# Performance work log

Measured on AMD Instinct MI355X. Metric: run time of the kernel, lower is better.

## Reference

```python
import jax, jax.numpy as jnp
import numpy as np

N_NODES = 50000
N_EDGES = 800000
IN_DIM = 128
EMB = 64
EDGE_DIM = 6
N_LAYERS = 4
OUT_DIM = 1


def setup_inputs() -> dict:
    key = jax.random.key(0)
    ks = jax.random.split(key, 20)
    s = 0.05
    inp = {
        "x": jax.random.normal(ks[0], (N_NODES, IN_DIM), jnp.float32),
        "edge_index": jax.random.randint(ks[1], (2, N_EDGES), 0, N_NODES, jnp.int64),
        "edge_attr": jax.random.normal(ks[2], (N_EDGES, EDGE_DIM), jnp.float32),
        # input projection
        "lin_in_w": jax.random.normal(ks[3], (IN_DIM, EMB), jnp.float32) * s,
        "lin_in_b": jnp.zeros((EMB,), jnp.float32),
        # stacked per-layer MLP params: message MLP psi: (2*EMB+EDGE_DIM)->EMB->EMB
        "msg_w1": jax.random.normal(ks[4], (N_LAYERS, 2 * EMB + EDGE_DIM, EMB), jnp.float32) * s,
        "msg_b1": jnp.zeros((N_LAYERS, EMB), jnp.float32),
        "msg_w2": jax.random.normal(ks[5], (N_LAYERS, EMB, EMB), jnp.float32) * s,
        "msg_b2": jnp.zeros((N_LAYERS, EMB), jnp.float32),
        # update MLP phi: (2*EMB)->EMB->EMB
        "upd_w1": jax.random.normal(ks[6], (N_LAYERS, 2 * EMB, EMB), jnp.float32) * s,
        "upd_b1": jnp.zeros((N_LAYERS, EMB), jnp.float32),
        "upd_w2": jax.random.normal(ks[7], (N_LAYERS, EMB, EMB), jnp.float32) * s,
        "upd_b2": jnp.zeros((N_LAYERS, EMB), jnp.float32),
        # output head
        "pred_w": jax.random.normal(ks[8], (EMB, OUT_DIM), jnp.float32) * s,
        "pred_b": jnp.zeros((OUT_DIM,), jnp.float32),
    }
    return inp


def reference(x, edge_index, edge_attr, lin_in_w, lin_in_b,
              msg_w1, msg_b1, msg_w2, msg_b2,
              upd_w1, upd_b1, upd_w2, upd_b2,
              pred_w, pred_b):
    n = x.shape[0]
    src = edge_index[0]  # h_j: source nodes
    dst = edge_index[1]  # h_i: target nodes (aggregation index in PyG default flow)
    h = x @ lin_in_w + lin_in_b  # (n, EMB)
    n_layers = msg_w1.shape[0]
    for l in range(n_layers):
        # message: psi([h_i, h_j, e_ij])  -> (E, EMB)
        m = jnp.concatenate([h[dst], h[src], edge_attr], axis=-1)
        m = jax.nn.relu(m @ msg_w1[l] + msg_b1[l])
        m = jax.nn.relu(m @ msg_w2[l] + msg_b2[l])
        # aggregate: scatter-add over target nodes
        agg = jax.ops.segment_sum(m, dst, num_segments=n)
        # update: phi([h, m_i]) with residual connection (h = h + conv(h))
        u = jnp.concatenate([h, agg], axis=-1)
        u = jax.nn.relu(u @ upd_w1[l] + upd_b1[l])
        u = jax.nn.relu(u @ upd_w2[l] + upd_b2[l])
        h = h + u
    out = h @ pred_w + pred_b  # (n, OUT_DIM)
    return jnp.sum(out, axis=-2)  # (OUT_DIM,)
```

## Files before the change

kernel.cpp:

```cpp
#include <hip/hip_runtime.h>


typedef __attribute__((ext_vector_type(8))) short short8;
typedef __attribute__((ext_vector_type(4))) float float4v;

__device__ __forceinline__ unsigned short f2bf(float f) {
    unsigned int u = __float_as_uint(f);
    unsigned int r = u + 0x7fff + ((u >> 16) & 1);
    return (unsigned short)(r >> 16);
}
__device__ __forceinline__ float bf2f(unsigned short u) {
    return __uint_as_float(((unsigned int)u) << 16);
}

#define MFMA16(a, b, c) __builtin_amdgcn_mfma_f32_16x16x32_bf16(a, b, c, 0, 0, 0)

struct bfpair { short hi, lo; };
__device__ __forceinline__ bfpair wsplit(float wv) {
    bfpair p;
    unsigned short h = f2bf(wv);
    float hf = __uint_as_float(((unsigned int)h) << 16);
    p.hi = (short)h;
    p.lo = (short)f2bf(wv - hf);
    return p;
}

#define WP_TOTAL 106496
#define OFF_IN   0
#define OFF_PRE(l)  (8192  + (l) * 8192)
#define OFF_MW2(l)  (40960 + (l) * 4096)
#define OFF_UW1(l)  (57344 + (l) * 8192)
#define OFF_UW2(l)  (90112 + (l) * 4096)

__global__ __launch_bounds__(256) void k_wprep(const float* __restrict__ lin_w,
        const float* __restrict__ mw1, const float* __restrict__ mw2,
        const float* __restrict__ uw1, const float* __restrict__ uw2,
        unsigned short* __restrict__ H, unsigned short* __restrict__ L) {
    const int tid = blockIdx.x * 256 + threadIdx.x;
    if (tid >= WP_TOTAL) return;
    float val;
    if (tid < 8192) {
        int rem = tid;
        int nt = rem >> 11, kf = (rem >> 9) & 3;
        int lane = (rem >> 3) & 63, j = rem & 7;
        int k = kf * 32 + (lane >> 4) * 8 + j;
        val = lin_w[k * 64 + nt * 16 + (lane & 15)];
    } else if (tid < 40960) {
        int t = tid - 8192, layer = t >> 13, rem = t & 8191;
        int nt = rem >> 10, kf = (rem >> 9) & 1;
        int lane = (rem >> 3) & 63, j = rem & 7;
        int k = kf * 32 + (lane >> 4) * 8 + j;
        const float* w1 = mw1 + (size_t)layer * 134 * 64;
        val = (nt < 4) ? w1[k * 64 + nt * 16 + (lane & 15)]
                       : w1[(64 + k) * 64 + (nt - 4) * 16 + (lane & 15)];
    } else if (tid < 57344) {
        int t = tid - 40960, layer = t >> 12, rem = t & 4095;
        int nt = rem >> 10, kf = (rem >> 9) & 1;
        int lane = (rem >> 3) & 63, j = rem & 7;
        int k = kf * 32 + (lane >> 4) * 8 + j;
        val = mw2[(size_t)layer * 4096 + k * 64 + nt * 16 + (lane & 15)];
    } else if (tid < 90112) {
        int t = tid - 57344, layer = t >> 13, rem = t & 8191;
        int nt = rem >> 11, kf = (rem >> 9) & 3;
        int lane = (rem >> 3) & 63, j = rem & 7;
        int k = kf * 32 + (lane >> 4) * 8 + j;
        val = uw1[(size_t)layer * 8192 + k * 64 + nt * 16 + (lane & 15)];
    } else {
        int t = tid - 90112, layer = t >> 12, rem = t & 4095;
        int nt = rem >> 10, kf = (rem >> 9) & 1;
        int lane = (rem >> 3) & 63, j = rem & 7;
        int k = kf * 32 + (lane >> 4) * 8 + j;
        val = uw2[(size_t)layer * 4096 + k * 64 + nt * 16 + (lane & 15)];
    }
    bfpair p = wsplit(val);
    H[tid] = (unsigned short)p.hi;
    L[tid] = (unsigned short)p.lo;
}

#define LOADFRAG(dst, arr, nt, KF, kf) \
    dst = *(const short8*)&arr[((((nt) * (KF)) + (kf)) * 64 + lane) * 8]

__global__ __launch_bounds__(256) void k_hist(const int* __restrict__ dst,
        int* __restrict__ deg, int nEdges) {
    int e = blockIdx.x * blockDim.x + threadIdx.x;
    if (e < nEdges) atomicAdd(&deg[dst[e]], 1);
}

__global__ __launch_bounds__(256) void k_scan1(const int* __restrict__ deg,
        int* __restrict__ local, int* __restrict__ bsum, int nNodes) {
    __shared__ int sm[256];
    const int t = threadIdx.x;
    const int n = blockIdx.x * 256 + t;
    int v = (n < nNodes) ? deg[n] : 0;
    sm[t] = v;
    __syncthreads();
    for (int off = 1; off < 256; off <<= 1) {
        int u = (t >= off) ? sm[t - off] : 0;
        __syncthreads();
        sm[t] += u;
        __syncthreads();
    }
    if (n < nNodes) local[n] = sm[t] - v;
    if (t == 255) bsum[blockIdx.x] = sm[255];
}

__global__ __launch_bounds__(256) void k_scan2(int* __restrict__ bsum, int nB) {
    __shared__ int sm[256];
    const int t = threadIdx.x;
    int v = (t < nB) ? bsum[t] : 0;
    sm[t] = v;
    __syncthreads();
    for (int off = 1; off < 256; off <<= 1) {
        int u = (t >= off) ? sm[t - off] : 0;
        __syncthreads();
        sm[t] += u;
        __syncthreads();
    }
    if (t < nB) bsum[t] = sm[t] - v;
}

__global__ __launch_bounds__(256) void k_scan3(const int* __restrict__ local,
        const int* __restrict__ bsum, int* __restrict__ cursor, int nNodes) {
    int n = blockIdx.x * 256 + threadIdx.x;
    if (n < nNodes) cursor[n] = bsum[blockIdx.x] + local[n];
}

__global__ __launch_bounds__(256) void k_scatter(const int* __restrict__ src,
        const int* __restrict__ dst, const float* __restrict__ ea,
        int* __restrict__ cursor, int* __restrict__ col_src,
        int* __restrict__ dst_s, float* __restrict__ ea_s, int nEdges) {
    int e = blockIdx.x * blockDim.x + threadIdx.x;
    if (e < nEdges) {
        int d = dst[e];
        int pos = atomicAdd(&cursor[d], 1);
        col_src[pos] = src[e];
        dst_s[pos] = d;
        const float* p = ea + (size_t)e * 6;
        float* q = ea_s + (size_t)pos * 6;
#pragma unroll
        for (int j = 0; j < 6; ++j) q[j] = p[j];
    }
}


__global__ __launch_bounds__(256) void k_in(const float* __restrict__ x,
        const unsigned short* __restrict__ wh, const unsigned short* __restrict__ wl,
        const float* __restrict__ bia, float* __restrict__ h, int nNodes) {
    const int lane = threadIdx.x & 63;
    const int wib  = threadIdx.x >> 6;
    const int quad = lane >> 4, col = lane & 15;
    __shared__ unsigned short sm[4][16 * 136];
    unsigned short* __restrict__ mt = sm[wib];

    short8 bh[4][4], bl[4][4];
#pragma unroll
    for (int nt = 0; nt < 4; ++nt)
#pragma unroll
        for (int kf = 0; kf < 4; ++kf) {
            LOADFRAG(bh[nt][kf], wh, nt, 4, kf);
            LOADFRAG(bl[nt][kf], wl, nt, 4, kf);
        }
    float bv[4];
#pragma unroll
    for (int nt = 0; nt < 4; ++nt) bv[nt] = bia[nt * 16 + col];

    const int nTiles = (nNodes + 15) >> 4;
    const int wid = blockIdx.x * 4 + wib;
    const int nw  = gridDim.x * 4;
    for (int tile = wid; tile < nTiles; tile += nw) {
        const int base = tile * 16;
#pragma unroll
        for (int j = 0; j < 16; ++j) {
            int row = min(base + j, nNodes - 1);
            mt[j * 136 + lane]      = f2bf(x[(size_t)row * 128 + lane]);
            mt[j * 136 + 64 + lane] = f2bf(x[(size_t)row * 128 + 64 + lane]);
        }
        __builtin_amdgcn_s_waitcnt(0);
        short8 a[4];
#pragma unroll
        for (int kf = 0; kf < 4; ++kf)
            a[kf] = *(const short8*)&mt[col * 136 + kf * 32 + quad * 8];
#pragma unroll
        for (int nt = 0; nt < 4; ++nt) {
            float4v c = {0.f, 0.f, 0.f, 0.f};
#pragma unroll
            for (int kf = 0; kf < 4; ++kf) c = MFMA16(a[kf], bh[nt][kf], c);
#pragma unroll
            for (int kf = 0; kf < 4; ++kf) c = MFMA16(a[kf], bl[nt][kf], c);
#pragma unroll
            for (int r = 0; r < 4; ++r) {
                int row = base + quad * 4 + r;
                if (row < nNodes)
                    h[(size_t)row * 64 + nt * 16 + col] = c[r] + bv[nt];
            }
        }
    }
}

__global__ __launch_bounds__(256) void k_pre(const float* __restrict__ h,
        const unsigned short* __restrict__ wh, const unsigned short* __restrict__ wl,
        const float* __restrict__ b1m,
        unsigned short* __restrict__ P, unsigned short* __restrict__ Q,
        int nNodes) {
    const int lane = threadIdx.x & 63;
    const int wib  = threadIdx.x >> 6;
    const int quad = lane >> 4, col = lane & 15;
    __shared__ unsigned short sm[4][16 * 72];
    unsigned short* __restrict__ mt = sm[wib];

    short8 bh[8][2], bl[8][2];
#pragma unroll
    for (int nt = 0; nt < 8; ++nt)
#pragma unroll
        for (int kf = 0; kf < 2; ++kf) {
            LOADFRAG(bh[nt][kf], wh, nt, 2, kf);
            LOADFRAG(bl[nt][kf], wl, nt, 2, kf);
        }
    float bv1[4];
#pragma unroll
    for (int nt = 0; nt < 4; ++nt) bv1[nt] = b1m[nt * 16 + col];

    const int nTiles = (nNodes + 15) >> 4;
    const int wid = blockIdx.x * 4 + wib;
    const int nw  = gridDim.x * 4;
    for (int tile = wid; tile < nTiles; tile += nw) {
        const int base = tile * 16;
#pragma unroll
        for (int j = 0; j < 16; ++j) {
            int row = min(base + j, nNodes - 1);
            mt[j * 72 + lane] = f2bf(h[(size_t)row * 64 + lane]);
        }
        __builtin_amdgcn_s_waitcnt(0);
        short8 a0 = *(const short8*)&mt[col * 72 + quad * 8];
        short8 a1 = *(const short8*)&mt[col * 72 + 32 + quad * 8];
#pragma unroll
        for (int nt = 0; nt < 8; ++nt) {
            float4v c = {0.f, 0.f, 0.f, 0.f};
            c = MFMA16(a0, bh[nt][0], c);
            c = MFMA16(a1, bh[nt][1], c);
            c = MFMA16(a0, bl[nt][0], c);
            c = MFMA16(a1, bl[nt][1], c);
            unsigned short* __restrict__ outp = (nt < 4) ? P : Q;
            const int nc = (nt & 3) * 16 + col;
            const float badd = (nt < 4) ? bv1[nt & 3] : 0.f;
#pragma unroll
            for (int r = 0; r < 4; ++r) {
                int row = base + quad * 4 + r;
                if (row < nNodes) outp[(size_t)row * 64 + nc] = f2bf(c[r] + badd);
            }
        }
    }
}

__global__ __launch_bounds__(256) void k_upd1(const float* __restrict__ h,
        const float* __restrict__ agg,
        const unsigned short* __restrict__ wh, const unsigned short* __restrict__ wl,
        const float* __restrict__ b1, float* __restrict__ tv, int nNodes) {
    const int lane = threadIdx.x & 63;
    const int wib  = threadIdx.x >> 6;
    const int quad = lane >> 4, col = lane & 15;
    __shared__ unsigned short sm[4][16 * 136];
    unsigned short* __restrict__ mt = sm[wib];

    short8 bh[4][4], bl[4][4];
#pragma unroll
    for (int nt = 0; nt < 4; ++nt)
#pragma unroll
        for (int kf = 0; kf < 4; ++kf) {
            LOADFRAG(bh[nt][kf], wh, nt, 4, kf);
            LOADFRAG(bl[nt][kf], wl, nt, 4, kf);
        }
    float bv[4];
#pragma unroll
    for (int nt = 0; nt < 4; ++nt) bv[nt] = b1[nt * 16 + col];

    const int nTiles = (nNodes + 15) >> 4;
    const int wid = blockIdx.x * 4 + wib;
    const int nw  = gridDim.x * 4;
    for (int tile = wid; tile < nTiles; tile += nw) {
        const int base = tile * 16;
#pragma unroll
        for (int j = 0; j < 16; ++j) {
            int row = min(base + j, nNodes - 1);
            mt[j * 136 + lane]      = f2bf(h[(size_t)row * 64 + lane]);
            mt[j * 136 + 64 + lane] = f2bf(agg[(size_t)row * 64 + lane]);
        }
        __builtin_amdgcn_s_waitcnt(0);
        short8 a[4];
#pragma unroll
        for (int kf = 0; kf < 4; ++kf)
            a[kf] = *(const short8*)&mt[col * 136 + kf * 32 + quad * 8];
#pragma unroll
        for (int nt = 0; nt < 4; ++nt) {
            float4v c = {0.f, 0.f, 0.f, 0.f};
#pragma unroll
            for (int kf = 0; kf < 4; ++kf) c = MFMA16(a[kf], bh[nt][kf], c);
#pragma unroll
            for (int kf = 0; kf < 4; ++kf) c = MFMA16(a[kf], bl[nt][kf], c);
#pragma unroll
            for (int r = 0; r < 4; ++r) {
                int row = base + quad * 4 + r;
                if (row < nNodes)
                    tv[(size_t)row * 64 + nt * 16 + col] = fmaxf(c[r] + bv[nt], 0.f);
            }
        }
    }
}

__global__ __launch_bounds__(256) void k_upd2(float* __restrict__ h,
        float* __restrict__ tv,
        const unsigned short* __restrict__ wh, const unsigned short* __restrict__ wl,
        const float* __restrict__ b2, float* __restrict__ colsum,
        int nNodes, int doCS) {
    const int lane = threadIdx.x & 63;
    const int wib  = threadIdx.x >> 6;
    const int quad = lane >> 4, col = lane & 15;
    __shared__ unsigned short sm[4][16 * 72];
    unsigned short* __restrict__ mt = sm[wib];

    short8 bh[4][2], bl[4][2];
#pragma unroll
    for (int nt = 0; nt < 4; ++nt)
#pragma unroll
        for (int kf = 0; kf < 2; ++kf) {
            LOADFRAG(bh[nt][kf], wh, nt, 2, kf);
            LOADFRAG(bl[nt][kf], wl, nt, 2, kf);
        }
    float bv[4];
#pragma unroll
    for (int nt = 0; nt < 4; ++nt) bv[nt] = b2[nt * 16 + col];

    float cs0 = 0.f, cs1 = 0.f, cs2 = 0.f, cs3 = 0.f;
    const int nTiles = (nNodes + 15) >> 4;
    const int wid = blockIdx.x * 4 + wib;
    const int nw  = gridDim.x * 4;
    for (int tile = wid; tile < nTiles; tile += nw) {
        const int base = tile * 16;
#pragma unroll
        for (int j = 0; j < 16; ++j) {
            int row = min(base + j, nNodes - 1);
            mt[j * 72 + lane] = f2bf(tv[(size_t)row * 64 + lane]);
        }
        __builtin_amdgcn_s_waitcnt(0);
#pragma unroll
        for (int j = 0; j < 16; ++j) {
            int row = base + j;
            if (row < nNodes) tv[(size_t)row * 64 + lane] = 0.f;
        }
        short8 a0 = *(const short8*)&mt[col * 72 + quad * 8];
        short8 a1 = *(const short8*)&mt[col * 72 + 32 + quad * 8];
#pragma unroll
        for (int nt = 0; nt < 4; ++nt) {
            float4v c = {0.f, 0.f, 0.f, 0.f};
            c = MFMA16(a0, bh[nt][0], c);
            c = MFMA16(a1, bh[nt][1], c);
            c = MFMA16(a0, bl[nt][0], c);
            c = MFMA16(a1, bl[nt][1], c);
#pragma unroll
            for (int r = 0; r < 4; ++r) {
                int row = base + quad * 4 + r;
                if (row < nNodes) {
                    float* hp = &h[(size_t)row * 64 + nt * 16 + col];
                    float hn = *hp + fmaxf(c[r] + bv[nt], 0.f);
                    *hp = hn;
                    cs0 += (nt == 0) ? hn : 0.f;
                    cs1 += (nt == 1) ? hn : 0.f;
                    cs2 += (nt == 2) ? hn : 0.f;
                    cs3 += (nt == 3) ? hn : 0.f;
                }
            }
        }
    }
    if (doCS) {
        cs0 += __shfl_xor(cs0, 16); cs0 += __shfl_xor(cs0, 32);
        cs1 += __shfl_xor(cs1, 16); cs1 += __shfl_xor(cs1, 32);
        cs2 += __shfl_xor(cs2, 16); cs2 += __shfl_xor(cs2, 32);
        cs3 += __shfl_xor(cs3, 16); cs3 += __shfl_xor(cs3, 32);
        const float tot = (quad == 0) ? cs0 : (quad == 1) ? cs1
                        : (quad == 2) ? cs2 : cs3;
        atomicAdd(&colsum[lane], tot);
    }
}

#define EST 72

__global__ __launch_bounds__(256, 4) void k_edge(const unsigned short* __restrict__ P,
        const unsigned short* __restrict__ Q, const float* __restrict__ ea_s,
        const int* __restrict__ col_src, const int* __restrict__ dst_s,
        const float* __restrict__ w1e,
        const unsigned short* __restrict__ wh, const unsigned short* __restrict__ wl,
        const float* __restrict__ b2,
        float* __restrict__ agg, int nEdges) {
    const int lane = threadIdx.x & 63;
    const int wib  = threadIdx.x >> 6;
    const int wid  = blockIdx.x * 4 + wib;
    const int nw   = gridDim.x * 4;
    const int quad = lane >> 4;
    const int col  = lane & 15;
    const int li   = lane & 31;

    __shared__ unsigned short m1b[4][32 * EST];
    __shared__ unsigned short wB[8192];
    unsigned short* __restrict__ mt = m1b[wib];

    {
        const short8* __restrict__ sH = (const short8*)wh;
        const short8* __restrict__ sL = (const short8*)wl;
        short8* __restrict__ dB = (short8*)wB;
        for (int i = threadIdx.x; i < 512; i += 256) {
            dB[i]       = sH[i];
            dB[512 + i] = sL[i];
        }
    }
    __syncthreads();

    float w1ec[6];
#pragma unroll
    for (int j = 0; j < 6; ++j) w1ec[j] = w1e[j * 64 + lane];

    float b2v[4];
#pragma unroll
    for (int nt = 0; nt < 4; ++nt) b2v[nt] = b2[nt * 16 + col];

    const int nBatch = (nEdges + 31) >> 5;
    const int per = nBatch / nw, rem = nBatch % nw;
    const int btLo = wid * per + min(wid, rem);
    const int btHi = btLo + per + (wid < rem ? 1 : 0);

    for (int bt = btLo; bt < btHi; ++bt) {
        const int base = __builtin_amdgcn_readfirstlane(bt << 5);
        const int gidx = min(base + li, nEdges - 1);
        const int vdj = dst_s[gidx];
        const int vsj = col_src[gidx];
        const int vprev = __shfl_up(vdj, 1);
        unsigned long long bmask =
            __ballot(lane < 32 && (li == 0 || vdj != vprev));
        bmask |= (1ull << 32) | 1ull;

#pragma unroll
        for (int j = 0; j < 32; ++j) {
            const int d = __builtin_amdgcn_readlane(vdj, j);
            const int s = __builtin_amdgcn_readlane(vsj, j);
            const int idx = min(base + j, nEdges - 1);
            float t = bf2f(P[(size_t)d * 64 + lane]) +
                      bf2f(Q[(size_t)s * 64 + lane]);
            const float* eap = ea_s + (size_t)idx * 6;
#pragma unroll
            for (int jj = 0; jj < 6; ++jj) t = fmaf(eap[jj], w1ec[jj], t);
            mt[j * EST + lane] = f2bf(fmaxf(t, 0.f));
        }
        __builtin_amdgcn_s_waitcnt(0);

        short8 a00 = *(const short8*)&mt[col * EST + quad * 8];
        short8 a01 = *(const short8*)&mt[col * EST + 32 + quad * 8];
        short8 a10 = *(const short8*)&mt[(16 + col) * EST + quad * 8];
        short8 a11 = *(const short8*)&mt[(16 + col) * EST + 32 + quad * 8];

        float4v m2v[2][4];
#pragma unroll
        for (int nt = 0; nt < 4; ++nt) {
            const short8 h0 = *(const short8*)&wB[((nt * 2 + 0) * 64 + lane) * 8];
            const short8 h1 = *(const short8*)&wB[((nt * 2 + 1) * 64 + lane) * 8];
            const short8 l0 = *(const short8*)&wB[4096 + ((nt * 2 + 0) * 64 + lane) * 8];
            const short8 l1 = *(const short8*)&wB[4096 + ((nt * 2 + 1) * 64 + lane) * 8];
            float4v c0 = {0.f, 0.f, 0.f, 0.f};
            float4v c1 = {0.f, 0.f, 0.f, 0.f};
            c0 = MFMA16(a00, h0, c0);
            c0 = MFMA16(a01, h1, c0);
            c0 = MFMA16(a00, l0, c0);
            c0 = MFMA16(a01, l1, c0);
            c1 = MFMA16(a10, h0, c1);
            c1 = MFMA16(a11, h1, c1);
            c1 = MFMA16(a10, l0, c1);
            c1 = MFMA16(a11, l1, c1);
#pragma unroll
            for (int r = 0; r < 4; ++r) {
                const bool v0 = base + (quad * 4 + r) < nEdges;
                const bool v1 = base + 16 + (quad * 4 + r) < nEdges;
                m2v[0][nt][r] = v0 ? fmaxf(c0[r] + b2v[nt], 0.f) : 0.f;
                m2v[1][nt][r] = v1 ? fmaxf(c1[r] + b2v[nt], 0.f) : 0.f;
            }
        }

        int r0 = 0;
        while (r0 < 32) {
            const int nid = __builtin_amdgcn_readlane(vdj, r0);
            const int r1 = r0 + 1 + (int)__builtin_ctzll(bmask >> (r0 + 1));
            float s0 = 0.f, s1 = 0.f, s2 = 0.f, s3 = 0.f;
#pragma unroll
            for (int t = 0; t < 2; ++t)
#pragma unroll
                for (int r = 0; r < 4; ++r) {
                    const int R = t * 16 + quad * 4 + r;
                    const bool in = (R >= r0) && (R < r1);
                    s0 += in ? m2v[t][0][r] : 0.f;
                    s1 += in ? m2v[t][1][r] : 0.f;
                    s2 += in ? m2v[t][2][r] : 0.f;
                    s3 += in ? m2v[t][3][r] : 0.f;
                }
            s0 += __shfl_xor(s0, 16); s0 += __shfl_xor(s0, 32);
            s1 += __shfl_xor(s1, 16); s1 += __shfl_xor(s1, 32);
            s2 += __shfl_xor(s2, 16); s2 += __shfl_xor(s2, 32);
            s3 += __shfl_xor(s3, 16); s3 += __shfl_xor(s3, 32);
            const float tot = (quad == 0) ? s0 : (quad == 1) ? s1
                            : (quad == 2) ? s2 : s3;
            atomicAdd(&agg[(size_t)nid * 64 + lane], tot);
            r0 = r1;
        }
    }
}

__global__ void k_out(const float* __restrict__ colsum, const float* __restrict__ pw,
                      const float* __restrict__ pb, float* __restrict__ out, int nNodes) {
    const int lane = threadIdx.x;
    float v = colsum[lane] * pw[lane];
#pragma unroll
    for (int off = 32; off; off >>= 1) v += __shfl_down(v, off);
    if (lane == 0) out[0] = v + (float)nNodes * pb[0];
}

extern "C" void kernel_launch(void* const* d_in, const int* in_sizes, int n_in,
                              void* d_out, int out_size, void* d_ws, size_t ws_size,
                              hipStream_t stream) {
    const float* x     = (const float*)d_in[0];
    const int*   ei    = (const int*)d_in[1];
    const float* ea    = (const float*)d_in[2];
    const float* lin_w = (const float*)d_in[3];
    const float* lin_b = (const float*)d_in[4];
    const float* mw1   = (const float*)d_in[5];
    const float* mb1   = (const float*)d_in[6];
    const float* mw2   = (const float*)d_in[7];
    const float* mb2   = (const float*)d_in[8];
    const float* uw1   = (const float*)d_in[9];
    const float* ub1   = (const float*)d_in[10];
    const float* uw2   = (const float*)d_in[11];
    const float* ub2   = (const float*)d_in[12];
    const float* pw    = (const float*)d_in[13];
    const float* pb    = (const float*)d_in[14];

    const int nNodes = in_sizes[0] / 128;
    const int nEdges = in_sizes[1] / 2;
    const int* src = ei;
    const int* dst = ei + nEdges;

    float* h       = (float*)d_ws;
    float* agg     = h   + (size_t)nNodes * 64;
    float* ea_s    = agg + (size_t)nNodes * 64;
    float* colsum  = ea_s + (size_t)nEdges * 6;
    unsigned short* Pb  = (unsigned short*)(colsum + 64);
    unsigned short* Qb  = Pb + (size_t)nNodes * 64;
    unsigned short* wpH = Qb + (size_t)nNodes * 64;
    unsigned short* wpL = wpH + WP_TOTAL;
    int*   deg     = (int*)(wpL + WP_TOTAL);
    int*   cursor  = deg + nNodes;
    int*   local   = cursor + nNodes;
    int*   bsum    = local + nNodes;
    int*   col_src = bsum + 256;
    int*   dst_s   = col_src + nEdges;

    const int NB_T    = 392;
    const int NB_EDGE = 2048;
    const int NB_FLAT = (nEdges + 255) / 256;
    const int NB_SCAN = (nNodes + 255) / 256;

    hipMemsetAsync(deg, 0, (size_t)nNodes * sizeof(int), stream);
    hipMemsetAsync(colsum, 0, 64 * sizeof(float), stream);
    hipMemsetAsync(agg, 0, (size_t)nNodes * 64 * sizeof(float), stream);
    k_hist<<<NB_FLAT, 256, 0, stream>>>(dst, deg, nEdges);
    k_scan1<<<NB_SCAN, 256, 0, stream>>>(deg, local, bsum, nNodes);
    k_scan2<<<1, 256, 0, stream>>>(bsum, NB_SCAN);
    k_scan3<<<NB_SCAN, 256, 0, stream>>>(local, bsum, cursor, nNodes);
    k_scatter<<<NB_FLAT, 256, 0, stream>>>(src, dst, ea, cursor, col_src, dst_s, ea_s, nEdges);
    k_wprep<<<(WP_TOTAL + 255) / 256, 256, 0, stream>>>(lin_w, mw1, mw2, uw1, uw2, wpH, wpL);

    k_in<<<NB_T, 256, 0, stream>>>(x, wpH + OFF_IN, wpL + OFF_IN, lin_b, h, nNodes);

    for (int l = 0; l < 4; ++l) {
        k_pre<<<NB_T, 256, 0, stream>>>(h, wpH + OFF_PRE(l), wpL + OFF_PRE(l),
            mb1 + l * 64, Pb, Qb, nNodes);
        k_edge<<<NB_EDGE, 256, 0, stream>>>(Pb, Qb, ea_s, col_src, dst_s,
            mw1 + (size_t)l * 134 * 64 + 128 * 64,
            wpH + OFF_MW2(l), wpL + OFF_MW2(l), mb2 + l * 64, agg, nEdges);
        k_upd1<<<NB_T, 256, 0, stream>>>(h, agg,
            wpH + OFF_UW1(l), wpL + OFF_UW1(l), ub1 + l * 64, agg, nNodes);
        k_upd2<<<NB_T, 256, 0, stream>>>(h, agg,
            wpH + OFF_UW2(l), wpL + OFF_UW2(l), ub2 + l * 64,
            colsum, nNodes, (l == 3) ? 1 : 0);
    }

    k_out<<<1, 64, 0, stream>>>(colsum, pw, pb, (float*)d_out, nNodes);
}
```

Baseline: 642.0 us.

## Switch edge message stage to packed fp16 math and fp16 MFMA

Stores the P/Q node projections and the second message-layer weights (hi/lo split) in fp16 instead of bf16, and computes the first message layer with packed half2 adds and FMAs. Each lane now handles two channels for two edges per iteration, halving the gather loop trip count. Edge attributes are staged in LDS as half2 per wave, and the second message GEMM uses the fp16 MFMA. This cuts VALU work and per-edge scalar loads in the edge kernel, at the cost of fp16 range and precision limits on the intermediate activations.

```diff
diff --git a/kernel.cpp b/kernel.cpp
--- a/kernel.cpp
+++ b/kernel.cpp
@@ -1,4 +1,5 @@
 #include <hip/hip_runtime.h>
+#include <hip/hip_fp16.h>
 
 
 typedef __attribute__((ext_vector_type(8))) short short8;
@@ -12,8 +13,20 @@
 __device__ __forceinline__ float bf2f(unsigned short u) {
     return __uint_as_float(((unsigned int)u) << 16);
 }
-
-#define MFMA16(a, b, c) __builtin_amdgcn_mfma_f32_16x16x32_bf16(a, b, c, 0, 0, 0)
+__device__ __forceinline__ __half2 u2h2(unsigned int u) {
+    union { unsigned int u; __half2 h; } c; c.u = u; return c.h;
+}
+__device__ __forceinline__ unsigned int h22u(__half2 h) {
+    union { unsigned int u; __half2 h; } c; c.h = h; return c.u;
+}
+__device__ __forceinline__ unsigned int pkmax0(unsigned int a) {
+    unsigned int r;
+    asm("v_pk_max_f16 %0, %1, %2" : "=v"(r) : "v"(a), "v"(0u));
+    return r;
+}
+
+#define MFMA16(a, b, c)  __builtin_amdgcn_mfma_f32_16x16x32_bf16(a, b, c, 0, 0, 0)
+#define MFMA16H(a, b, c) __builtin_amdgcn_mfma_f32_16x16x32_f16(a, b, c, 0, 0, 0)
 
 struct bfpair { short hi, lo; };
 __device__ __forceinline__ bfpair wsplit(float wv) {
@@ -72,9 +85,17 @@
         int k = kf * 32 + (lane >> 4) * 8 + j;
         val = uw2[(size_t)layer * 4096 + k * 64 + nt * 16 + (lane & 15)];
     }
-    bfpair p = wsplit(val);
-    H[tid] = (unsigned short)p.hi;
-    L[tid] = (unsigned short)p.lo;
+    if (tid >= 40960 && tid < 57344) {
+        __half hh = __float2half_rn(val);
+        float hf = __half2float(hh);
+        __half hl = __float2half_rn(val - hf);
+        H[tid] = __half_as_ushort(hh);
+        L[tid] = __half_as_ushort(hl);
+    } else {
+        bfpair p = wsplit(val);
+        H[tid] = (unsigned short)p.hi;
+        L[tid] = (unsigned short)p.lo;
+    }
 }
 
 #define LOADFRAG(dst, arr, nt, KF, kf) \
@@ -246,7 +267,9 @@
 #pragma unroll
             for (int r = 0; r < 4; ++r) {
                 int row = base + quad * 4 + r;
-                if (row < nNodes) outp[(size_t)row * 64 + nc] = f2bf(c[r] + badd);
+                if (row < nNodes)
+                    outp[(size_t)row * 64 + nc] =
+                        __half_as_ushort(__float2half_rn(c[r] + badd));
             }
         }
     }
@@ -398,10 +421,13 @@
     const int quad = lane >> 4;
     const int col  = lane & 15;
     const int li   = lane & 31;
+    const int hs   = lane >> 5;
 
     __shared__ unsigned short m1b[4][32 * EST];
+    __shared__ unsigned int   eab[4][192];
     __shared__ unsigned short wB[8192];
-    unsigned short* __restrict__ mt = m1b[wib];
+    unsigned short* __restrict__ mt  = m1b[wib];
+    unsigned int*   __restrict__ eaw = eab[wib];
 
     {
         const short8* __restrict__ sH = (const short8*)wh;
@@ -414,9 +440,11 @@
     }
     __syncthreads();
 
-    float w1ec[6];
-#pragma unroll
-    for (int j = 0; j < 6; ++j) w1ec[j] = w1e[j * 64 + lane];
+    __half2 w1ec2[6];
+#pragma unroll
+    for (int jj = 0; jj < 6; ++jj)
+        w1ec2[jj] = __halves2half2(__float2half_rn(w1e[jj * 64 + 2 * li]),
+                                   __float2half_rn(w1e[jj * 64 + 2 * li + 1]));
 
     float b2v[4];
 #pragma unroll
@@ -437,17 +465,26 @@
             __ballot(lane < 32 && (li == 0 || vdj != vprev));
         bmask |= (1ull << 32) | 1ull;
 
-#pragma unroll
-        for (int j = 0; j < 32; ++j) {
-            const int d = __builtin_amdgcn_readlane(vdj, j);
-            const int s = __builtin_amdgcn_readlane(vsj, j);
-            const int idx = min(base + j, nEdges - 1);
-            float t = bf2f(P[(size_t)d * 64 + lane]) +
-                      bf2f(Q[(size_t)s * 64 + lane]);
-            const float* eap = ea_s + (size_t)idx * 6;
-#pragma unroll
-            for (int jj = 0; jj < 6; ++jj) t = fmaf(eap[jj], w1ec[jj], t);
-            mt[j * EST + lane] = f2bf(fmaxf(t, 0.f));
+        const int eaMax = nEdges * 6 - 1;
+        const int eaBase = base * 6;
+        eaw[lane]       = h22u(__float2half2_rn(ea_s[min(eaBase + lane,       eaMax)]));
+        eaw[64 + lane]  = h22u(__float2half2_rn(ea_s[min(eaBase + 64 + lane,  eaMax)]));
+        eaw[128 + lane] = h22u(__float2half2_rn(ea_s[min(eaBase + 128 + lane, eaMax)]));
+
+#pragma unroll
+        for (int j = 0; j < 16; ++j) {
+            const int rsel = 2 * j + hs;
+            const int d = __shfl(vdj, rsel);
+            const int s = __shfl(vsj, rsel);
+            const unsigned int p2 = *(const unsigned int*)&P[(size_t)d * 64 + 2 * li];
+            const unsigned int q2 = *(const unsigned int*)&Q[(size_t)s * 64 + 2 * li];
+            __half2 t = __hadd2(u2h2(p2), u2h2(q2));
+#pragma unroll
+            for (int jj = 0; jj < 6; ++jj) {
+                const unsigned int eu = eaw[12 * j + jj + 6 * hs];
+                t = __hfma2(u2h2(eu), w1ec2[jj], t);
+            }
+            *(unsigned int*)((char*)mt + rsel * (EST * 2) + li * 4) = pkmax0(h22u(t));
         }
         __builtin_amdgcn_s_waitcnt(0);
 
@@ -465,14 +502,14 @@
             const short8 l1 = *(const short8*)&wB[4096 + ((nt * 2 + 1) * 64 + lane) * 8];
             float4v c0 = {0.f, 0.f, 0.f, 0.f};
             float4v c1 = {0.f, 0.f, 0.f, 0.f};
-            c0 = MFMA16(a00, h0, c0);
-            c0 = MFMA16(a01, h1, c0);
-            c0 = MFMA16(a00, l0, c0);
-            c0 = MFMA16(a01, l1, c0);
-            c1 = MFMA16(a10, h0, c1);
-            c1 = MFMA16(a11, h1, c1);
-            c1 = MFMA16(a10, l0, c1);
-            c1 = MFMA16(a11, l1, c1);
+            c0 = MFMA16H(a00, h0, c0);
+            c0 = MFMA16H(a01, h1, c0);
+            c0 = MFMA16H(a00, l0, c0);
+            c0 = MFMA16H(a01, l1, c0);
+            c1 = MFMA16H(a10, h0, c1);
+            c1 = MFMA16H(a11, h1, c1);
+            c1 = MFMA16H(a10, l0, c1);
+            c1 = MFMA16H(a11, l1, c1);
 #pragma unroll
             for (int r = 0; r < 4; ++r) {
                 const bool v0 = base + (quad * 4 + r) < nEdges;
```

New measurement: 694.7 us. 1.08x slower.
